# Kernel tuning notes

Hardware: AMD Instinct MI355X
Metric: run time of the kernel (lower is better)

## Reference

```python
import jax, jax.numpy as jnp
import numpy as np

N_NODES = 50000
N_REL = 3
N_EDGES = 500000
D_IN, D_HID, D_OUT = 128, 256, 128


def setup_inputs() -> dict:
    key = jax.random.key(0)
    ks = jax.random.split(key, 9)
    def w(k, shape, fan_in):
        return jax.random.normal(k, shape, dtype=jnp.float32) / np.sqrt(fan_in)
    return {
        "x": jax.random.normal(ks[0], (N_NODES, D_IN), dtype=jnp.float32),
        "src": jax.random.randint(ks[1], (N_REL, N_EDGES), 0, N_NODES, dtype=jnp.int32),
        "dst": jax.random.randint(ks[2], (N_REL, N_EDGES), 0, N_NODES, dtype=jnp.int32),
        "w_self1": w(ks[3], (N_REL, D_IN, D_HID), D_IN),
        "w_neigh1": w(ks[4], (N_REL, D_IN, D_HID), D_IN),
        "b1": jnp.zeros((N_REL, D_HID), dtype=jnp.float32),
        "w_self2": w(ks[5], (N_REL, D_HID, D_OUT), D_HID),
        "w_neigh2": w(ks[6], (N_REL, D_HID, D_OUT), D_HID),
        "b2": jnp.zeros((N_REL, D_OUT), dtype=jnp.float32),
    }


def _sage_hetero_layer(x, src, dst, w_self, w_neigh, b):
    """Multi-relation SAGEConv (mean agg); relation outputs summed (HeteroGraphConv default).
    x: [N, din]; src/dst: [R, E]; w_*: [R, din, dout]; b: [R, dout]."""
    n = x.shape[0]

    def per_rel(s, d, ws, wn, bb):
        gathered = jnp.take(x, s, axis=0)                      # [E, din] neighbor gather
        summed = jax.ops.segment_sum(gathered, d, num_segments=n)  # [N, din]
        deg = jax.ops.segment_sum(jnp.ones(s.shape, jnp.float32), d, num_segments=n)
        h_neigh = summed / jnp.maximum(deg, 1.0)[:, None]      # mean, 0 for isolated dst
        return x @ ws + h_neigh @ wn + bb                      # fc_self + fc_neigh + bias

    per_rel_out = jax.vmap(per_rel)(src, dst, w_self, w_neigh, b)  # [R, N, dout]
    return per_rel_out.sum(axis=0)


def reference(x, src, dst, w_self1, w_neigh1, b1, w_self2, w_neigh2, b2):
    h = _sage_hetero_layer(x, src, dst, w_self1, w_neigh1, b1)
    h = jax.nn.relu(h)  # SAGEConv activation in hidden layers
    out = _sage_hetero_layer(h, src, dst, w_self2, w_neigh2, b2)  # last layer: no activation
    return out
```

## Files before the change

kernel.cpp:

```cpp
#include <hip/hip_runtime.h>

#define NN 50000
#define NREL 3
#define NE 500000
#define DIN 128
#define DHID 256
#define DOUT 128

#define NBUK 98
#define CAP 8192
#define EPB 2048
#define NCHK ((NE + EPB - 1) / EPB)

typedef unsigned int uint;
typedef unsigned short ushort;
typedef __attribute__((ext_vector_type(8))) short bf16x8;
typedef __attribute__((ext_vector_type(4))) float f32x4;

using gptr_t = const __attribute__((address_space(1))) unsigned int*;
using lptr_t = __attribute__((address_space(3))) unsigned int*;

__device__ __forceinline__ ushort f2bf(float f) {
    uint u = __float_as_uint(f);
    uint r = (u + 0x7fffu + ((u >> 16) & 1u)) >> 16;
    return (ushort)r;
}
__device__ __forceinline__ float bflo(uint u) { return __uint_as_float(u << 16); }
__device__ __forceinline__ float bfhi(uint u) { return __uint_as_float(u & 0xffff0000u); }

__global__ __launch_bounds__(256) void pass_a(const int* __restrict__ src,
                                              const int* __restrict__ dst,
                                              int* __restrict__ bcursor,
                                              uint* __restrict__ pairs) {
    int r = blockIdx.x / NCHK;
    int chunk = blockIdx.x % NCHK;
    int e0 = chunk * EPB;
    int nedge = min(EPB, NE - e0);
    const int* S = src + (size_t)r * NE + e0;
    const int* D = dst + (size_t)r * NE + e0;
    __shared__ int cnt[NBUK], base[NBUK], cur[NBUK];
    int tid = threadIdx.x;
    if (tid < NBUK) { cnt[tid] = 0; cur[tid] = 0; }
    __syncthreads();
    uint pk[8];
    int bk[8];
    bool val[8];
#pragma unroll
    for (int j = 0; j < 8; ++j) {
        int e = j * 256 + tid;
        val[j] = e < nedge;
        int d = val[j] ? D[e] : 0;
        int s = val[j] ? S[e] : 0;
        bk[j] = d >> 9;
        pk[j] = ((uint)s << 9) | (uint)(d & 511);
        if (val[j]) atomicAdd(&cnt[bk[j]], 1);
    }
    __syncthreads();
    if (tid < NBUK) base[tid] = atomicAdd(&bcursor[r * NBUK + tid], cnt[tid]);
    __syncthreads();
#pragma unroll
    for (int j = 0; j < 8; ++j) {
        if (val[j]) {
            int slot = base[bk[j]] + atomicAdd(&cur[bk[j]], 1);
            if (slot < CAP) pairs[(size_t)(r * NBUK + bk[j]) * CAP + slot] = pk[j];
        }
    }
}

__global__ __launch_bounds__(256) void bucket_scan(const int* __restrict__ bcnt,
                                                   int* __restrict__ boffs) {
    __shared__ int sc[256];
    int tid = threadIdx.x;
    int i0 = 2 * tid, i1 = 2 * tid + 1;
    int v0 = (i0 < NREL * NBUK) ? bcnt[i0] : 0;
    int v1 = (i1 < NREL * NBUK) ? bcnt[i1] : 0;
    int s = v0 + v1;
    sc[tid] = s;
    __syncthreads();
    for (int st = 1; st < 256; st <<= 1) {
        int t = (tid >= st) ? sc[tid - st] : 0;
        __syncthreads();
        sc[tid] += t;
        __syncthreads();
    }
    int excl = sc[tid] - s;
    if (i0 < NREL * NBUK) boffs[i0] = excl;
    if (i1 < NREL * NBUK) boffs[i1] = excl + v0;
}

__global__ __launch_bounds__(256) void pass_b(const uint* __restrict__ pairs,
                                              const int* __restrict__ bcnt,
                                              const int* __restrict__ boffs,
                                              int* __restrict__ srclist,
                                              int* __restrict__ deg,
                                              int* __restrict__ offs) {
    int blk = blockIdx.x;
    int b = blk % NBUK;
    int r = blk / NBUK;
    int node_base = b * 512;
    int count = min(bcnt[blk], CAP);
    int obase = boffs[blk];
    const uint* pp = pairs + (size_t)blk * CAP;
    __shared__ int hist[512];
    __shared__ int cur[512];
    __shared__ int sc[256];
    int tid = threadIdx.x;
    hist[tid] = 0;
    hist[tid + 256] = 0;
    __syncthreads();
    for (int i = tid; i < count; i += 256) atomicAdd(&hist[pp[i] & 511], 1);
    __syncthreads();
    int v0 = hist[2 * tid], v1 = hist[2 * tid + 1];
    int s = v0 + v1;
    sc[tid] = s;
    __syncthreads();
    for (int st = 1; st < 256; st <<= 1) {
        int t = (tid >= st) ? sc[tid - st] : 0;
        __syncthreads();
        sc[tid] += t;
        __syncthreads();
    }
    int excl = sc[tid] - s;
    int c0 = obase + excl;
    int c1 = c0 + v0;
    cur[2 * tid] = c0;
    cur[2 * tid + 1] = c1;
    int n0 = node_base + 2 * tid;
    if (n0 < NN)     { deg[r * NN + n0] = v0;     offs[r * NN + n0] = c0; }
    if (n0 + 1 < NN) { deg[r * NN + n0 + 1] = v1; offs[r * NN + n0 + 1] = c1; }
    __syncthreads();
    for (int i = tid; i < count; i += 256) {
        uint p = pp[i];
        int pos = atomicAdd(&cur[p & 511], 1);
        srclist[pos] = (int)(p >> 9);
    }
}

__global__ __launch_bounds__(256) void sum3_kernel(const float* __restrict__ in,
                                                   float* __restrict__ out, int sz) {
    int t = blockIdx.x * 256 + threadIdx.x;
    if (t < sz) out[t] = in[t] + in[sz + t] + in[2 * sz + t];
}

__global__ __launch_bounds__(256) void f2bf_vec_kernel(const float* __restrict__ in,
                                                       ushort* __restrict__ out, int n4) {
    int t = blockIdx.x * 256 + threadIdx.x;
    if (t >= n4) return;
    float4 v = *(const float4*)(in + (size_t)t * 4);
    uint2 p;
    p.x = (uint)f2bf(v.x) | ((uint)f2bf(v.y) << 16);
    p.y = (uint)f2bf(v.z) | ((uint)f2bf(v.w) << 16);
    *(uint2*)(out + (size_t)t * 4) = p;
}

__global__ __launch_bounds__(256) void pack_b1(const float* __restrict__ ws1,
                                               const float* __restrict__ wn1,
                                               ushort* __restrict__ Bt1) {
    int t = blockIdx.x * 256 + threadIdx.x;
    if (t >= 256 * 512) return;
    int n = t >> 9, k = t & 511;
    int b = k >> 7, kk = k & 127;
    float v;
    if (b == 0)
        v = ws1[kk * 256 + n] + ws1[128 * 256 + kk * 256 + n] + ws1[2 * 128 * 256 + kk * 256 + n];
    else
        v = wn1[(size_t)(b - 1) * 128 * 256 + kk * 256 + n];
    Bt1[t] = f2bf(v);
}

__global__ __launch_bounds__(256) void pack_b2(const float* __restrict__ ws2,
                                               const float* __restrict__ wn2,
                                               ushort* __restrict__ Bt2) {
    int t = blockIdx.x * 256 + threadIdx.x;
    if (t >= 512 * 256) return;
    int n = t >> 8, k = t & 255;
    int c = n >> 7, j = n & 127;
    float v;
    if (c == 0)
        v = ws2[k * 128 + j] + ws2[256 * 128 + k * 128 + j] + ws2[2 * 256 * 128 + k * 128 + j];
    else
        v = wn2[(size_t)(c - 1) * 256 * 128 + k * 128 + j];
    Bt2[t] = f2bf(v);
}

template <int PHASE>
__global__ __launch_bounds__(256) void gather3(
    const ushort* __restrict__ f0, const ushort* __restrict__ f1,
    const ushort* __restrict__ f2, const int* __restrict__ offs,
    const int* __restrict__ deg, const int* __restrict__ srclist,
    ushort* __restrict__ ob, float* __restrict__ of) {
    int node = blockIdx.x * 4 + (threadIdx.x >> 6);
    if (node >= NN) return;
    int lane = threadIdx.x & 63;
    int g = lane >> 4, c = lane & 15;
    float msum[8];
#pragma unroll
    for (int k = 0; k < 8; ++k) msum[k] = 0.f;

    for (int r = 0; r < NREL; ++r) {
        const ushort* feat = (r == 0) ? f0 : (r == 1) ? f1 : f2;
        int beg = offs[r * NN + node];
        int d = deg[r * NN + node];
        float acc[8];
#pragma unroll
        for (int k = 0; k < 8; ++k) acc[k] = 0.f;

        for (int i = 0; i < d; i += 64) {
            int sid_l = (i + lane < d) ? srclist[beg + i + lane] : 0;
            int m = (d - i < 64) ? (d - i) : 64;
            for (int j0 = 0; j0 < m; j0 += 4) {
                int jj = j0 + g;
                int sid = __shfl(sid_l, (jj < m) ? jj : 0);
                if (jj < m) {
                    uint4 v = *(const uint4*)(feat + (size_t)sid * 128 + c * 8);
                    acc[0] += bflo(v.x); acc[1] += bfhi(v.x);
                    acc[2] += bflo(v.y); acc[3] += bfhi(v.y);
                    acc[4] += bflo(v.z); acc[5] += bfhi(v.z);
                    acc[6] += bflo(v.w); acc[7] += bfhi(v.w);
                }
            }
        }
#pragma unroll
        for (int k = 0; k < 8; ++k) {
            acc[k] += __shfl_xor(acc[k], 16);
            acc[k] += __shfl_xor(acc[k], 32);
        }
        float inv = 1.f / fmaxf((float)d, 1.f);
        if (PHASE == 0) {
            if (g == 0) {
                uint4 pk;
                pk.x = (uint)f2bf(acc[0] * inv) | ((uint)f2bf(acc[1] * inv) << 16);
                pk.y = (uint)f2bf(acc[2] * inv) | ((uint)f2bf(acc[3] * inv) << 16);
                pk.z = (uint)f2bf(acc[4] * inv) | ((uint)f2bf(acc[5] * inv) << 16);
                pk.w = (uint)f2bf(acc[6] * inv) | ((uint)f2bf(acc[7] * inv) << 16);
                *(uint4*)(ob + (size_t)r * NN * DIN + (size_t)node * 128 + c * 8) = pk;
            }
        } else {
#pragma unroll
            for (int k = 0; k < 8; ++k) msum[k] += acc[k] * inv;
        }
    }
    if (PHASE == 1 && g == 0) {
        float* po = of + (size_t)node * 128 + c * 8;
        float4 a = *(float4*)po;
        float4 b = *(float4*)(po + 4);
        a.x += msum[0]; a.y += msum[1]; a.z += msum[2]; a.w += msum[3];
        b.x += msum[4]; b.y += msum[5]; b.z += msum[6]; b.w += msum[7];
        *(float4*)po = a;
        *(float4*)(po + 4) = b;
    }
}

template <int LAYER>
__global__ __launch_bounds__(256) void gemm_mfma(
    const ushort* __restrict__ A0, const ushort* __restrict__ A1,
    const ushort* __restrict__ A2, const ushort* __restrict__ A3,
    const ushort* __restrict__ Bt, const float* __restrict__ bias,
    ushort* __restrict__ HO, float* __restrict__ CO,
    ushort* __restrict__ Y1, ushort* __restrict__ Y2, ushort* __restrict__ Y3) {
    constexpr int KTOT = (LAYER == 1) ? 512 : 256;
    constexpr int ASTRIDE = (LAYER == 1) ? 128 : 256;
    __shared__ __align__(16) ushort As[128 * 32];
    __shared__ __align__(16) ushort Bs[128 * 32];

    const int tid = threadIdx.x, lane = tid & 63, w = tid >> 6;
    const int wr = w >> 1, wc = w & 1;
    const int bm = blockIdx.x * 128;
    const int bn = blockIdx.y * 128;

    f32x4 acc[4][4];
#pragma unroll
    for (int m = 0; m < 4; ++m)
#pragma unroll
        for (int n = 0; n < 4; ++n) acc[m][n] = (f32x4){0.f, 0.f, 0.f, 0.f};

    const int arow = lane >> 2;
    const int akq = (lane & 3) * 8;

    for (int k0 = 0; k0 < KTOT; k0 += 32) {
        const ushort* Ab = A0;
        int koff = k0;
        if (LAYER == 1) {
            int b = k0 >> 7;
            Ab = (b == 0) ? A0 : (b == 1) ? A1 : (b == 2) ? A2 : A3;
            koff = k0 & 127;
        }
#pragma unroll
        for (int i = 0; i < 2; ++i) {
            int c = w + i * 4;
            const ushort* srcA = Ab + (size_t)(bm + c * 16 + arow) * ASTRIDE + koff + akq;
            __builtin_amdgcn_global_load_lds((gptr_t)srcA, (lptr_t)(As + c * 512), 16, 0, 0);
            const ushort* srcB = Bt + (size_t)(bn + c * 16 + arow) * KTOT + k0 + akq;
            __builtin_amdgcn_global_load_lds((gptr_t)srcB, (lptr_t)(Bs + c * 512), 16, 0, 0);
        }
        __syncthreads();

        const int r = lane & 15, g = lane >> 4;
        bf16x8 af[4], bg[4];
#pragma unroll
        for (int m = 0; m < 4; ++m)
            af[m] = *(const bf16x8*)&As[(wr * 64 + m * 16 + r) * 32 + g * 8];
#pragma unroll
        for (int n = 0; n < 4; ++n)
            bg[n] = *(const bf16x8*)&Bs[(wc * 64 + n * 16 + r) * 32 + g * 8];
#pragma unroll
        for (int m = 0; m < 4; ++m)
#pragma unroll
            for (int n = 0; n < 4; ++n)
                acc[m][n] = __builtin_amdgcn_mfma_f32_16x16x32_bf16(af[m], bg[n], acc[m][n], 0, 0, 0);
        __syncthreads();
    }

    const int r = lane & 15, g = lane >> 4;
    if (LAYER == 1) {
#pragma unroll
        for (int m = 0; m < 4; ++m)
#pragma unroll
            for (int v = 0; v < 4; ++v) {
                int gm = bm + wr * 64 + m * 16 + g * 4 + v;
                if (gm >= NN) continue;
#pragma unroll
                for (int n = 0; n < 4; ++n) {
                    int gn = bn + wc * 64 + n * 16 + r;
                    float f = acc[m][n][v] + bias[gn];
                    f = fmaxf(f, 0.f);
                    HO[(size_t)gm * 256 + gn] = f2bf(f);
                }
            }
    } else {
        if (blockIdx.y == 0) {
#pragma unroll
            for (int m = 0; m < 4; ++m)
#pragma unroll
                for (int v = 0; v < 4; ++v) {
                    int gm = bm + wr * 64 + m * 16 + g * 4 + v;
                    if (gm >= NN) continue;
#pragma unroll
                    for (int n = 0; n < 4; ++n) {
                        int gn = wc * 64 + n * 16 + r;
                        CO[(size_t)gm * 128 + gn] = acc[m][n][v] + bias[gn];
                    }
                }
        } else {
            ushort* Y = (blockIdx.y == 1) ? Y1 : (blockIdx.y == 2) ? Y2 : Y3;
#pragma unroll
            for (int m = 0; m < 4; ++m)
#pragma unroll
                for (int v = 0; v < 4; ++v) {
                    int gm = bm + wr * 64 + m * 16 + g * 4 + v;
                    if (gm >= NN) continue;
#pragma unroll
                    for (int n = 0; n < 4; ++n) {
                        int gn = wc * 64 + n * 16 + r;
                        Y[(size_t)gm * 128 + gn] = f2bf(acc[m][n][v]);
                    }
                }
        }
    }
}

extern "C" void kernel_launch(void* const* d_in, const int* in_sizes, int n_in,
                              void* d_out, int out_size, void* d_ws, size_t ws_size,
                              hipStream_t stream) {
    const float* x        = (const float*)d_in[0];
    const int*   src      = (const int*)d_in[1];
    const int*   dst      = (const int*)d_in[2];
    const float* w_self1  = (const float*)d_in[3];
    const float* w_neigh1 = (const float*)d_in[4];
    const float* b1       = (const float*)d_in[5];
    const float* w_self2  = (const float*)d_in[6];
    const float* w_neigh2 = (const float*)d_in[7];
    const float* b2       = (const float*)d_in[8];
    float* out = (float*)d_out;

    char* ws = (char*)d_ws;
    size_t off = 0;
    auto alloc = [&](size_t bytes) {
        char* p = ws + off;
        off += (bytes + 255) & ~(size_t)255;
        return p;
    };
    int*    bcursor = (int*)alloc(NREL * NBUK * 4);
    int*    boffs   = (int*)alloc(NREL * NBUK * 4);
    int*    deg     = (int*)alloc(NREL * NN * 4);
    int*    offs    = (int*)alloc(NREL * NN * 4);
    int*    srclist = (int*)alloc((size_t)NREL * NE * 4);
    float*  bsum1   = (float*)alloc(DHID * 4);
    float*  bsum2   = (float*)alloc(DOUT * 4);
    ushort* Bt1     = (ushort*)alloc((size_t)DHID * 512 * 2);
    ushort* Bt2     = (ushort*)alloc((size_t)512 * DHID * 2);
    ushort* xb      = (ushort*)alloc((size_t)NN * DIN * 2);
    ushort* aggb    = (ushort*)alloc((size_t)NREL * NN * DIN * 2);
    ushort* Hb      = (ushort*)alloc((size_t)NN * DHID * 2);
    (void)alloc(65536);
    uint* pairs = (uint*)Hb;

    hipMemsetAsync(bcursor, 0, NREL * NBUK * 4, stream);
    pass_a<<<NREL * NCHK, 256, 0, stream>>>(src, dst, bcursor, pairs);
    bucket_scan<<<1, 256, 0, stream>>>(bcursor, boffs);
    pass_b<<<NREL * NBUK, 256, 0, stream>>>(pairs, bcursor, boffs, srclist, deg, offs);

    f2bf_vec_kernel<<<(NN * DIN / 4 + 255) / 256, 256, 0, stream>>>(x, xb, NN * DIN / 4);
    sum3_kernel<<<1, 256, 0, stream>>>(b1, bsum1, DHID);
    sum3_kernel<<<1, 256, 0, stream>>>(b2, bsum2, DOUT);
    pack_b1<<<(256 * 512 + 255) / 256, 256, 0, stream>>>(w_self1, w_neigh1, Bt1);
    pack_b2<<<(512 * 256 + 255) / 256, 256, 0, stream>>>(w_self2, w_neigh2, Bt2);

    int ggrid = (NN + 3) / 4;

    gather3<0><<<ggrid, 256, 0, stream>>>(xb, xb, xb, offs, deg, srclist, aggb, nullptr);
    {
        dim3 grid((NN + 127) / 128, DHID / 128);
        gemm_mfma<1><<<grid, 256, 0, stream>>>(
            xb, aggb, aggb + (size_t)NN * DIN, aggb + (size_t)2 * NN * DIN,
            Bt1, bsum1, Hb, nullptr, nullptr, nullptr, nullptr);
    }
    {
        dim3 grid((NN + 127) / 128, 4);
        gemm_mfma<2><<<grid, 256, 0, stream>>>(
            Hb, nullptr, nullptr, nullptr, Bt2, bsum2,
            nullptr, out, aggb, aggb + (size_t)NN * DIN, aggb + (size_t)2 * NN * DIN);
    }
    gather3<1><<<ggrid, 256, 0, stream>>>(
        aggb, aggb + (size_t)NN * DIN, aggb + (size_t)2 * NN * DIN,
        offs, deg, srclist, nullptr, out);
}
```

Before: 262.6 us.

## Fuse prep kernels, drop bucket scan, widen GEMM tiles, unroll gather

Several independent changes. The bucket prefix scan is removed by giving each bucket a fixed CAP-sized slot in srclist, and the cast, weight-pack and bias-sum kernels are merged into one prep launch. This cuts launch overhead at the cost of a larger, sparser srclist. The gather loop now issues two neighbor row loads per iteration for more memory parallelism. The GEMM uses 512-thread blocks with 128x256 tiles so the A tile is loaded once per block for all output columns.

```diff
diff --git a/kernel.cpp b/kernel.cpp
--- a/kernel.cpp
+++ b/kernel.cpp
@@ -25,8 +25,10 @@
     uint r = (u + 0x7fffu + ((u >> 16) & 1u)) >> 16;
     return (ushort)r;
 }
-__device__ __forceinline__ float bflo(uint u) { return __uint_as_float(u << 16); }
-__device__ __forceinline__ float bfhi(uint u) { return __uint_as_float(u & 0xffff0000u); }
+__device__ __forceinline__ void acc2(float2& a, uint u) {
+    a.x += __uint_as_float(u << 16);
+    a.y += __uint_as_float(u & 0xffff0000u);
+}
 
 __global__ __launch_bounds__(256) void pass_a(const int* __restrict__ src,
                                               const int* __restrict__ dst,
@@ -67,30 +69,8 @@
     }
 }
 
-__global__ __launch_bounds__(256) void bucket_scan(const int* __restrict__ bcnt,
-                                                   int* __restrict__ boffs) {
-    __shared__ int sc[256];
-    int tid = threadIdx.x;
-    int i0 = 2 * tid, i1 = 2 * tid + 1;
-    int v0 = (i0 < NREL * NBUK) ? bcnt[i0] : 0;
-    int v1 = (i1 < NREL * NBUK) ? bcnt[i1] : 0;
-    int s = v0 + v1;
-    sc[tid] = s;
-    __syncthreads();
-    for (int st = 1; st < 256; st <<= 1) {
-        int t = (tid >= st) ? sc[tid - st] : 0;
-        __syncthreads();
-        sc[tid] += t;
-        __syncthreads();
-    }
-    int excl = sc[tid] - s;
-    if (i0 < NREL * NBUK) boffs[i0] = excl;
-    if (i1 < NREL * NBUK) boffs[i1] = excl + v0;
-}
-
 __global__ __launch_bounds__(256) void pass_b(const uint* __restrict__ pairs,
                                               const int* __restrict__ bcnt,
-                                              const int* __restrict__ boffs,
                                               int* __restrict__ srclist,
                                               int* __restrict__ deg,
                                               int* __restrict__ offs) {
@@ -99,7 +79,7 @@
     int r = blk / NBUK;
     int node_base = b * 512;
     int count = min(bcnt[blk], CAP);
-    int obase = boffs[blk];
+    int obase = blk * CAP;
     const uint* pp = pairs + (size_t)blk * CAP;
     __shared__ int hist[512];
     __shared__ int cur[512];
@@ -136,51 +116,45 @@
     }
 }
 
-__global__ __launch_bounds__(256) void sum3_kernel(const float* __restrict__ in,
-                                                   float* __restrict__ out, int sz) {
-    int t = blockIdx.x * 256 + threadIdx.x;
-    if (t < sz) out[t] = in[t] + in[sz + t] + in[2 * sz + t];
-}
-
-__global__ __launch_bounds__(256) void f2bf_vec_kernel(const float* __restrict__ in,
-                                                       ushort* __restrict__ out, int n4) {
-    int t = blockIdx.x * 256 + threadIdx.x;
-    if (t >= n4) return;
-    float4 v = *(const float4*)(in + (size_t)t * 4);
-    uint2 p;
-    p.x = (uint)f2bf(v.x) | ((uint)f2bf(v.y) << 16);
-    p.y = (uint)f2bf(v.z) | ((uint)f2bf(v.w) << 16);
-    *(uint2*)(out + (size_t)t * 4) = p;
-}
-
-__global__ __launch_bounds__(256) void pack_b1(const float* __restrict__ ws1,
-                                               const float* __restrict__ wn1,
-                                               ushort* __restrict__ Bt1) {
-    int t = blockIdx.x * 256 + threadIdx.x;
-    if (t >= 256 * 512) return;
-    int n = t >> 9, k = t & 511;
-    int b = k >> 7, kk = k & 127;
-    float v;
-    if (b == 0)
-        v = ws1[kk * 256 + n] + ws1[128 * 256 + kk * 256 + n] + ws1[2 * 128 * 256 + kk * 256 + n];
-    else
-        v = wn1[(size_t)(b - 1) * 128 * 256 + kk * 256 + n];
-    Bt1[t] = f2bf(v);
-}
-
-__global__ __launch_bounds__(256) void pack_b2(const float* __restrict__ ws2,
-                                               const float* __restrict__ wn2,
-                                               ushort* __restrict__ Bt2) {
-    int t = blockIdx.x * 256 + threadIdx.x;
-    if (t >= 512 * 256) return;
-    int n = t >> 8, k = t & 255;
-    int c = n >> 7, j = n & 127;
-    float v;
-    if (c == 0)
-        v = ws2[k * 128 + j] + ws2[256 * 128 + k * 128 + j] + ws2[2 * 256 * 128 + k * 128 + j];
-    else
-        v = wn2[(size_t)(c - 1) * 256 * 128 + k * 128 + j];
-    Bt2[t] = f2bf(v);
+#define F2B_BLKS 6250
+__global__ __launch_bounds__(256) void prep_kernel(
+    const float* __restrict__ x, ushort* __restrict__ xb,
+    const float* __restrict__ ws1, const float* __restrict__ wn1, ushort* __restrict__ Bt1,
+    const float* __restrict__ ws2, const float* __restrict__ wn2, ushort* __restrict__ Bt2,
+    const float* __restrict__ b1, float* __restrict__ bsum1,
+    const float* __restrict__ b2, float* __restrict__ bsum2) {
+    int blk = blockIdx.x, tid = threadIdx.x;
+    if (blk < F2B_BLKS) {
+        int t = blk * 256 + tid;
+        float4 v = *(const float4*)(x + (size_t)t * 4);
+        uint2 p;
+        p.x = (uint)f2bf(v.x) | ((uint)f2bf(v.y) << 16);
+        p.y = (uint)f2bf(v.z) | ((uint)f2bf(v.w) << 16);
+        *(uint2*)(xb + (size_t)t * 4) = p;
+    } else if (blk < F2B_BLKS + 512) {
+        int t = (blk - F2B_BLKS) * 256 + tid;
+        int n = t >> 9, k = t & 511;
+        int b = k >> 7, kk = k & 127;
+        float v;
+        if (b == 0)
+            v = ws1[kk * 256 + n] + ws1[128 * 256 + kk * 256 + n] + ws1[2 * 128 * 256 + kk * 256 + n];
+        else
+            v = wn1[(size_t)(b - 1) * 128 * 256 + kk * 256 + n];
+        Bt1[t] = f2bf(v);
+    } else if (blk < F2B_BLKS + 1024) {
+        int t = (blk - F2B_BLKS - 512) * 256 + tid;
+        int n = t >> 8, k = t & 255;
+        int c = n >> 7, j = n & 127;
+        float v;
+        if (c == 0)
+            v = ws2[k * 128 + j] + ws2[256 * 128 + k * 128 + j] + ws2[2 * 256 * 128 + k * 128 + j];
+        else
+            v = wn2[(size_t)(c - 1) * 256 * 128 + k * 128 + j];
+        Bt2[t] = f2bf(v);
+    } else {
+        if (tid < DHID) bsum1[tid] = b1[tid] + b1[DHID + tid] + b1[2 * DHID + tid];
+        if (tid < DOUT) bsum2[tid] = b2[tid] + b2[DOUT + tid] + b2[2 * DOUT + tid];
+    }
 }
 
 template <int PHASE>
@@ -193,66 +167,77 @@
     if (node >= NN) return;
     int lane = threadIdx.x & 63;
     int g = lane >> 4, c = lane & 15;
-    float msum[8];
-#pragma unroll
-    for (int k = 0; k < 8; ++k) msum[k] = 0.f;
+    float2 msum[4];
+#pragma unroll
+    for (int k = 0; k < 4; ++k) msum[k] = make_float2(0.f, 0.f);
 
     for (int r = 0; r < NREL; ++r) {
         const ushort* feat = (r == 0) ? f0 : (r == 1) ? f1 : f2;
         int beg = offs[r * NN + node];
         int d = deg[r * NN + node];
-        float acc[8];
-#pragma unroll
-        for (int k = 0; k < 8; ++k) acc[k] = 0.f;
-
-        for (int i = 0; i < d; i += 64) {
-            int sid_l = (i + lane < d) ? srclist[beg + i + lane] : 0;
-            int m = (d - i < 64) ? (d - i) : 64;
-            for (int j0 = 0; j0 < m; j0 += 4) {
-                int jj = j0 + g;
-                int sid = __shfl(sid_l, (jj < m) ? jj : 0);
-                if (jj < m) {
-                    uint4 v = *(const uint4*)(feat + (size_t)sid * 128 + c * 8);
-                    acc[0] += bflo(v.x); acc[1] += bfhi(v.x);
-                    acc[2] += bflo(v.y); acc[3] += bfhi(v.y);
-                    acc[4] += bflo(v.z); acc[5] += bfhi(v.z);
-                    acc[6] += bflo(v.w); acc[7] += bfhi(v.w);
+        float2 ac[4];
+#pragma unroll
+        for (int k = 0; k < 4; ++k) ac[k] = make_float2(0.f, 0.f);
+
+        for (int i0 = 0; i0 < d; i0 += 64) {
+            int m = d - i0;
+            if (m > 64) m = 64;
+            int sid_l = (lane < m) ? srclist[beg + i0 + lane] : 0;
+            for (int j0 = 0; j0 < m; j0 += 8) {
+                int j1 = j0 + g;
+                int j2 = j0 + 4 + g;
+                int s1 = __shfl(sid_l, (j1 < m) ? j1 : 0);
+                int s2 = __shfl(sid_l, (j2 < m) ? j2 : 0);
+                uint4 v1 = *(const uint4*)(feat + (size_t)s1 * 128 + c * 8);
+                uint4 v2 = *(const uint4*)(feat + (size_t)s2 * 128 + c * 8);
+                if (j1 < m) {
+                    acc2(ac[0], v1.x); acc2(ac[1], v1.y);
+                    acc2(ac[2], v1.z); acc2(ac[3], v1.w);
                 }
-            }
-        }
-#pragma unroll
-        for (int k = 0; k < 8; ++k) {
-            acc[k] += __shfl_xor(acc[k], 16);
-            acc[k] += __shfl_xor(acc[k], 32);
+                if (j2 < m) {
+                    acc2(ac[0], v2.x); acc2(ac[1], v2.y);
+                    acc2(ac[2], v2.z); acc2(ac[3], v2.w);
+                }
+            }
+        }
+#pragma unroll
+        for (int k = 0; k < 4; ++k) {
+            ac[k].x += __shfl_xor(ac[k].x, 16);
+            ac[k].y += __shfl_xor(ac[k].y, 16);
+            ac[k].x += __shfl_xor(ac[k].x, 32);
+            ac[k].y += __shfl_xor(ac[k].y, 32);
         }
         float inv = 1.f / fmaxf((float)d, 1.f);
         if (PHASE == 0) {
             if (g == 0) {
                 uint4 pk;
-                pk.x = (uint)f2bf(acc[0] * inv) | ((uint)f2bf(acc[1] * inv) << 16);
-                pk.y = (uint)f2bf(acc[2] * inv) | ((uint)f2bf(acc[3] * inv) << 16);
-                pk.z = (uint)f2bf(acc[4] * inv) | ((uint)f2bf(acc[5] * inv) << 16);
-                pk.w = (uint)f2bf(acc[6] * inv) | ((uint)f2bf(acc[7] * inv) << 16);
+                pk.x = (uint)f2bf(ac[0].x * inv) | ((uint)f2bf(ac[0].y * inv) << 16);
+                pk.y = (uint)f2bf(ac[1].x * inv) | ((uint)f2bf(ac[1].y * inv) << 16);
+                pk.z = (uint)f2bf(ac[2].x * inv) | ((uint)f2bf(ac[2].y * inv) << 16);
+                pk.w = (uint)f2bf(ac[3].x * inv) | ((uint)f2bf(ac[3].y * inv) << 16);
                 *(uint4*)(ob + (size_t)r * NN * DIN + (size_t)node * 128 + c * 8) = pk;
             }
         } else {
 #pragma unroll
-            for (int k = 0; k < 8; ++k) msum[k] += acc[k] * inv;
+            for (int k = 0; k < 4; ++k) {
+                msum[k].x += ac[k].x * inv;
+                msum[k].y += ac[k].y * inv;
+            }
         }
     }
     if (PHASE == 1 && g == 0) {
         float* po = of + (size_t)node * 128 + c * 8;
         float4 a = *(float4*)po;
         float4 b = *(float4*)(po + 4);
-        a.x += msum[0]; a.y += msum[1]; a.z += msum[2]; a.w += msum[3];
-        b.x += msum[4]; b.y += msum[5]; b.z += msum[6]; b.w += msum[7];
+        a.x += msum[0].x; a.y += msum[0].y; a.z += msum[1].x; a.w += msum[1].y;
+        b.x += msum[2].x; b.y += msum[2].y; b.z += msum[3].x; b.w += msum[3].y;
         *(float4*)po = a;
         *(float4*)(po + 4) = b;
     }
 }
 
 template <int LAYER>
-__global__ __launch_bounds__(256) void gemm_mfma(
+__global__ __launch_bounds__(512) void gemm_mfma(
     const ushort* __restrict__ A0, const ushort* __restrict__ A1,
     const ushort* __restrict__ A2, const ushort* __restrict__ A3,
     const ushort* __restrict__ Bt, const float* __restrict__ bias,
@@ -261,12 +246,12 @@
     constexpr int KTOT = (LAYER == 1) ? 512 : 256;
     constexpr int ASTRIDE = (LAYER == 1) ? 128 : 256;
     __shared__ __align__(16) ushort As[128 * 32];
-    __shared__ __align__(16) ushort Bs[128 * 32];
+    __shared__ __align__(16) ushort Bs[256 * 32];
 
     const int tid = threadIdx.x, lane = tid & 63, w = tid >> 6;
-    const int wr = w >> 1, wc = w & 1;
+    const int wr = w >> 2, wc = w & 3;
     const int bm = blockIdx.x * 128;
-    const int bn = blockIdx.y * 128;
+    const int bn = blockIdx.y * 256;
 
     f32x4 acc[4][4];
 #pragma unroll
@@ -274,8 +259,8 @@
 #pragma unroll
         for (int n = 0; n < 4; ++n) acc[m][n] = (f32x4){0.f, 0.f, 0.f, 0.f};
 
-    const int arow = lane >> 2;
-    const int akq = (lane & 3) * 8;
+    const int srow = tid >> 2;
+    const int schunk = (tid & 3) * 8;
 
     for (int k0 = 0; k0 < KTOT; k0 += 32) {
         const ushort* Ab = A0;
@@ -285,13 +270,15 @@
             Ab = (b == 0) ? A0 : (b == 1) ? A1 : (b == 2) ? A2 : A3;
             koff = k0 & 127;
         }
+        {
+            const ushort* srcA = Ab + (size_t)(bm + srow) * ASTRIDE + koff + schunk;
+            __builtin_amdgcn_global_load_lds((gptr_t)srcA, (lptr_t)(As + w * 512), 16, 0, 0);
+        }
 #pragma unroll
         for (int i = 0; i < 2; ++i) {
-            int c = w + i * 4;
-            const ushort* srcA = Ab + (size_t)(bm + c * 16 + arow) * ASTRIDE + koff + akq;
-            __builtin_amdgcn_global_load_lds((gptr_t)srcA, (lptr_t)(As + c * 512), 16, 0, 0);
-            const ushort* srcB = Bt + (size_t)(bn + c * 16 + arow) * KTOT + k0 + akq;
-            __builtin_amdgcn_global_load_lds((gptr_t)srcB, (lptr_t)(Bs + c * 512), 16, 0, 0);
+            int row = i * 128 + srow;
+            const ushort* srcB = Bt + (size_t)(bn + row) * KTOT + k0 + schunk;
+            __builtin_amdgcn_global_load_lds((gptr_t)srcB, (lptr_t)(Bs + i * 4096 + w * 512), 16, 0, 0);
         }
         __syncthreads();
 
@@ -321,41 +308,30 @@
                 if (gm >= NN) continue;
 #pragma unroll
                 for (int n = 0; n < 4; ++n) {
-                    int gn = bn + wc * 64 + n * 16 + r;
+                    int gn = wc * 64 + n * 16 + r;
                     float f = acc[m][n][v] + bias[gn];
                     f = fmaxf(f, 0.f);
                     HO[(size_t)gm * 256 + gn] = f2bf(f);
                 }
             }
     } else {
-        if (blockIdx.y == 0) {
-#pragma unroll
-            for (int m = 0; m < 4; ++m)
-#pragma unroll
-                for (int v = 0; v < 4; ++v) {
-                    int gm = bm + wr * 64 + m * 16 + g * 4 + v;
-                    if (gm >= NN) continue;
-#pragma unroll
-                    for (int n = 0; n < 4; ++n) {
-                        int gn = wc * 64 + n * 16 + r;
-                        CO[(size_t)gm * 128 + gn] = acc[m][n][v] + bias[gn];
-                    }
+        int buf = (bn >> 7) + (wc >> 1);
+        ushort* Y = (buf == 1) ? Y1 : (buf == 2) ? Y2 : Y3;
+#pragma unroll
+        for (int m = 0; m < 4; ++m)
+#pragma unroll
+            for (int v = 0; v < 4; ++v) {
+                int gm = bm + wr * 64 + m * 16 + g * 4 + v;
+                if (gm >= NN) continue;
+#pragma unroll
+                for (int n = 0; n < 4; ++n) {
+                    int col = (wc & 1) * 64 + n * 16 + r;
+                    if (buf == 0)
+                        CO[(size_t)gm * 128 + col] = acc[m][n][v] + bias[col];
+                    else
+                        Y[(size_t)gm * 128 + col] = f2bf(acc[m][n][v]);
                 }
-        } else {
-            ushort* Y = (blockIdx.y == 1) ? Y1 : (blockIdx.y == 2) ? Y2 : Y3;
-#pragma unroll
-            for (int m = 0; m < 4; ++m)
-#pragma unroll
-                for (int v = 0; v < 4; ++v) {
-                    int gm = bm + wr * 64 + m * 16 + g * 4 + v;
-                    if (gm >= NN) continue;
-#pragma unroll
-                    for (int n = 0; n < 4; ++n) {
-                        int gn = wc * 64 + n * 16 + r;
-                        Y[(size_t)gm * 128 + gn] = f2bf(acc[m][n][v]);
-                    }
-                }
-        }
+            }
     }
 }
 
@@ -381,10 +357,9 @@
         return p;
     };
     int*    bcursor = (int*)alloc(NREL * NBUK * 4);
-    int*    boffs   = (int*)alloc(NREL * NBUK * 4);
     int*    deg     = (int*)alloc(NREL * NN * 4);
     int*    offs    = (int*)alloc(NREL * NN * 4);
-    int*    srclist = (int*)alloc((size_t)NREL * NE * 4);
+    int*    srclist = (int*)alloc((size_t)NREL * NBUK * CAP * 4);
     float*  bsum1   = (float*)alloc(DHID * 4);
     float*  bsum2   = (float*)alloc(DOUT * 4);
     ushort* Bt1     = (ushort*)alloc((size_t)DHID * 512 * 2);
@@ -397,27 +372,23 @@
 
     hipMemsetAsync(bcursor, 0, NREL * NBUK * 4, stream);
     pass_a<<<NREL * NCHK, 256, 0, stream>>>(src, dst, bcursor, pairs);
-    bucket_scan<<<1, 256, 0, stream>>>(bcursor, boffs);
-    pass_b<<<NREL * NBUK, 256, 0, stream>>>(pairs, bcursor, boffs, srclist, deg, offs);
-
-    f2bf_vec_kernel<<<(NN * DIN / 4 + 255) / 256, 256, 0, stream>>>(x, xb, NN * DIN / 4);
-    sum3_kernel<<<1, 256, 0, stream>>>(b1, bsum1, DHID);
-    sum3_kernel<<<1, 256, 0, stream>>>(b2, bsum2, DOUT);
-    pack_b1<<<(256 * 512 + 255) / 256, 256, 0, stream>>>(w_self1, w_neigh1, Bt1);
-    pack_b2<<<(512 * 256 + 255) / 256, 256, 0, stream>>>(w_self2, w_neigh2, Bt2);
+    pass_b<<<NREL * NBUK, 256, 0, stream>>>(pairs, bcursor, srclist, deg, offs);
+
+    prep_kernel<<<F2B_BLKS + 1024 + 1, 256, 0, stream>>>(
+        x, xb, w_self1, w_neigh1, Bt1, w_self2, w_neigh2, Bt2, b1, bsum1, b2, bsum2);
 
     int ggrid = (NN + 3) / 4;
 
     gather3<0><<<ggrid, 256, 0, stream>>>(xb, xb, xb, offs, deg, srclist, aggb, nullptr);
     {
-        dim3 grid((NN + 127) / 128, DHID / 128);
-        gemm_mfma<1><<<grid, 256, 0, stream>>>(
+        dim3 grid((NN + 127) / 128, 1);
+        gemm_mfma<1><<<grid, 512, 0, stream>>>(
             xb, aggb, aggb + (size_t)NN * DIN, aggb + (size_t)2 * NN * DIN,
             Bt1, bsum1, Hb, nullptr, nullptr, nullptr, nullptr);
     }
     {
-        dim3 grid((NN + 127) / 128, 4);
-        gemm_mfma<2><<<grid, 256, 0, stream>>>(
+        dim3 grid((NN + 127) / 128, 2);
+        gemm_mfma<2><<<grid, 512, 0, stream>>>(
             Hb, nullptr, nullptr, nullptr, Bt2, bsum2,
             nullptr, out, aggb, aggb + (size_t)NN * DIN, aggb + (size_t)2 * NN * DIN);
     }
```

After: 243.7 us. 1.08x faster.
